# Kernel tuning notes

Hardware: AMD Instinct MI355X
Metric: run time of the kernel (lower is better)

Reference implementation:

```python
import jax, jax.numpy as jnp
import numpy as np

P = 16                     # patch size
D = 192                    # embed dim (forced by SAT d_model=192)
NHEAD = 3                  # ViT-Tiny heads
SAT_H, SAT_DK, SAT_DV = 8, 32, 32
N_SLICE = 10
PER_LI = jnp.linspace(0.1, 1.0, N_SLICE)
LN_EPS = 1e-5


def layernorm(z, g, b):
    m = z.mean(-1, keepdims=True)
    v = ((z - m) ** 2).mean(-1, keepdims=True)
    return (z - m) * jax.lax.rsqrt(v + LN_EPS) * g + b


def setup_inputs() -> dict:
    key = jax.random.key(0)
    ks = jax.random.split(key, 32)
    B, IMG, DEPTH, MLP = 128, 224, 12, 4 * D
    S = (IMG // P) ** 2 + 1  # 197 tokens
    n = lambda k, sh: jax.random.normal(k, sh, jnp.float32) * 0.02
    z = lambda sh: jnp.zeros(sh, jnp.float32)
    o = lambda sh: jnp.ones(sh, jnp.float32)
    return {
        "x": jax.random.uniform(ks[0], (B, 3, IMG, IMG), jnp.float32),
        "x_g_norm": jax.random.uniform(ks[1], (B, 1, 56, 56), jnp.float32),
        "patch_w": n(ks[2], (D, 3, P, P)), "patch_b": z((D,)),
        "cls_token": n(ks[3], (1, 1, D)), "pos_embed": n(ks[4], (1, S, D)),
        "eleva_embed": n(ks[5], (1, D)),
        "sat_wq": n(ks[6], (D, SAT_H * SAT_DK)), "sat_bq": z((SAT_H * SAT_DK,)),
        "sat_wk": n(ks[7], (D, SAT_H * SAT_DK)), "sat_bk": z((SAT_H * SAT_DK,)),
        "sat_wv": n(ks[8], (D, SAT_H * SAT_DV)), "sat_bv": z((SAT_H * SAT_DV,)),
        "sat_wo": n(ks[9], (SAT_H * SAT_DV, D)), "sat_bo": z((D,)),
        "ln1_g": o((DEPTH, D)), "ln1_b": z((DEPTH, D)),
        "qkv_w": n(ks[10], (DEPTH, D, 3 * D)), "qkv_b": z((DEPTH, 3 * D)),
        "proj_w": n(ks[11], (DEPTH, D, D)), "proj_b": z((DEPTH, D)),
        "ln2_g": o((DEPTH, D)), "ln2_b": z((DEPTH, D)),
        "fc1_w": n(ks[12], (DEPTH, D, MLP)), "fc1_b": z((DEPTH, MLP)),
        "fc2_w": n(ks[13], (DEPTH, MLP, D)), "fc2_b": z((DEPTH, D)),
        "norm_g": o((D,)), "norm_b": z((D,)),
    }


def _forward(x, x_g_norm, patch_w, patch_b, cls_token, pos_embed, eleva_embed,
             sat_wq, sat_bq, sat_wk, sat_bk, sat_wv, sat_bv, sat_wo, sat_bo,
             ln1_g, ln1_b, qkv_w, qkv_b, proj_w, proj_b, ln2_g, ln2_b,
             fc1_w, fc1_b, fc2_w, fc2_b, norm_g, norm_b):
    B = x.shape[0]
    # --- patch embed: Conv2d(3, D, kernel=P, stride=P) -> [B, N, D] ---
    feat = jax.lax.conv_general_dilated(
        x, patch_w, (P, P), 'VALID', dimension_numbers=('NCHW', 'OIHW', 'NCHW'))
    feat = feat + patch_b[None, :, None, None]
    tokens = feat.reshape(B, D, -1).transpose(0, 2, 1)          # [B, 196, D]
    tok = jnp.concatenate([jnp.broadcast_to(cls_token, (B, 1, D)), tokens], axis=1)
    tok = tok + pos_embed                                        # [B, S, D]
    S = tok.shape[1]
    # --- elevation weight per sample (vectorized bisect + linear interp) ---
    means = x_g_norm.mean(axis=(1, 2, 3))                        # [B]
    idx = jnp.clip(jnp.searchsorted(PER_LI, means, side='left'), 0, N_SLICE - 1)
    per_hi = PER_LI[idx]
    per_lo = jnp.where(idx == 0, 0.0, PER_LI[jnp.maximum(idx - 1, 0)])
    idx_f = idx.astype(jnp.float32)
    idx_inter = idx_f - (per_hi - means) / (per_hi - per_lo)
    w = jnp.where(idx == N_SLICE - 1, idx_f, idx_inter) / N_SLICE  # [B]
    # --- SAT fusion: per (batch, token) a 2-element attention over (token, ele) ---
    ele = jnp.broadcast_to(eleva_embed[0] * w[:, None, None], tok.shape)  # [B,S,D]
    at_in = jnp.stack([tok, ele], axis=2)                        # [B, S, 2, D]
    q = (at_in @ sat_wq + sat_bq).reshape(B, S, 2, SAT_H, SAT_DK)
    k = (at_in @ sat_wk + sat_bk).reshape(B, S, 2, SAT_H, SAT_DK)
    v = (at_in @ sat_wv + sat_bv).reshape(B, S, 2, SAT_H, SAT_DV)
    att = jnp.einsum('bsqhd,bskhd->bshqk', q, k) * (1.0 / np.sqrt(SAT_DK))
    att = jax.nn.softmax(att, axis=-1)
    sat_o = jnp.einsum('bshqk,bskhd->bsqhd', att, v).reshape(B, S, 2, SAT_H * SAT_DV)
    sat_o = sat_o @ sat_wo + sat_bo                              # [B, S, 2, D]
    h = sat_o[..., 0, :] + sat_o[..., 1, :]                      # [B, S, D]
    # --- ViT blocks via scan over stacked layer params ---
    hd = D // NHEAD

    def block(z, p):
        l1g, l1b, qw, qb, pw, pb, l2g, l2b, f1w, f1b, f2w, f2b = p
        y = layernorm(z, l1g, l1b)
        qkv = y @ qw + qb                                        # [B, S, 3D]
        q_, k_, v_ = jnp.split(qkv, 3, axis=-1)
        q_ = q_.reshape(B, S, NHEAD, hd)
        k_ = k_.reshape(B, S, NHEAD, hd)
        v_ = v_.reshape(B, S, NHEAD, hd)
        a = jnp.einsum('bqhd,bkhd->bhqk', q_, k_) * (hd ** -0.5)
        a = jax.nn.softmax(a, axis=-1)
        o = jnp.einsum('bhqk,bkhd->bqhd', a, v_).reshape(B, S, D)
        z = z + o @ pw + pb
        y = layernorm(z, l2g, l2b)
        z = z + jax.nn.gelu(y @ f1w + f1b, approximate=False) @ f2w + f2b
        return z, None

    h, _ = jax.lax.scan(block, h, (ln1_g, ln1_b, qkv_w, qkv_b, proj_w, proj_b,
                                   ln2_g, ln2_b, fc1_w, fc1_b, fc2_w, fc2_b))
    h = layernorm(h, norm_g, norm_b)
    return h[:, 0]                                               # [B, D] cls token


def reference(x, x_g_norm, patch_w, patch_b, cls_token, pos_embed, eleva_embed,
              sat_wq, sat_bq, sat_wk, sat_bk, sat_wv, sat_bv, sat_wo, sat_bo,
              ln1_g, ln1_b, qkv_w, qkv_b, proj_w, proj_b, ln2_g, ln2_b,
              fc1_w, fc1_b, fc2_w, fc2_b, norm_g, norm_b):
    return _forward(x, x_g_norm, patch_w, patch_b, cls_token, pos_embed, eleva_embed,
                    sat_wq, sat_bq, sat_wk, sat_bk, sat_wv, sat_bv, sat_wo, sat_bo,
                    ln1_g, ln1_b, qkv_w, qkv_b, proj_w, proj_b, ln2_g, ln2_b,
                    fc1_w, fc1_b, fc2_w, fc2_b, norm_g, norm_b)
```

## Files before the change

kernel.cpp:

```cpp
#include <hip/hip_runtime.h>


#define BATCH 128
#define SEQ 197
#define BS_ROWS (BATCH * SEQ)
#define DMODEL 192
#define NPATCH 196
#define MROWS_PATCH (BATCH * NPATCH)
#define KPATCH 768
#define MLPDIM 768
#define DEPTH 12
#define SPAD 224

typedef float f32x4 __attribute__((ext_vector_type(4)));
typedef short s16x8 __attribute__((ext_vector_type(8)));

__device__ __forceinline__ float wredSum(float v) {
#pragma unroll
  for (int o = 32; o > 0; o >>= 1) v += __shfl_xor(v, o, 64);
  return v;
}

__device__ __forceinline__ unsigned short f2bf(float f) {
  union { float f; unsigned u; } v;
  v.f = f;
  unsigned r = v.u + 0x7FFFu + ((v.u >> 16) & 1u);
  return (unsigned short)(r >> 16);
}
__device__ __forceinline__ float bf2f(unsigned short u) {
  union { unsigned u; float f; } v;
  v.u = ((unsigned)u) << 16;
  return v.f;
}

__global__ __launch_bounds__(256) void eleva_w_kernel(const float* __restrict__ xg,
                                                      float* __restrict__ wout) {
  const int b = blockIdx.x;
  const float* p = xg + (size_t)b * 3136;
  float s = 0.f;
  for (int i = threadIdx.x; i < 3136; i += 256) s += p[i];
  __shared__ float partial[4];
  s = wredSum(s);
  if ((threadIdx.x & 63) == 0) partial[threadIdx.x >> 6] = s;
  __syncthreads();
  if (threadIdx.x == 0) {
    float m = (partial[0] + partial[1] + partial[2] + partial[3]) / 3136.f;
    int idx = 0;
#pragma unroll
    for (int i = 0; i < 10; i++) {
      float pv = 0.1f * (float)(i + 1);
      if (pv < m) idx = i + 1;
    }
    if (idx > 9) idx = 9;
    float wv;
    if (idx == 9) {
      wv = 9.f;
    } else {
      float hi = 0.1f * (float)(idx + 1);
      float lo = (idx == 0) ? 0.f : 0.1f * (float)idx;
      wv = (float)idx - (hi - m) / (hi - lo);
    }
    wout[b] = wv / 10.f;
  }
}

__global__ __launch_bounds__(256) void wtrans_kernel(const float* __restrict__ in,
                                                     unsigned short* __restrict__ out,
                                                     int R, int C) {
  const int z = blockIdx.z;
  in += (size_t)z * R * C;
  out += (size_t)z * R * C;
  const int c0 = blockIdx.x * 32, r0 = blockIdx.y * 32;
  __shared__ float t[32][33];
  const int tr = threadIdx.x >> 3, tc = (threadIdx.x & 7) * 4;
  const float4 v = *(const float4*)(in + (size_t)(r0 + tr) * C + c0 + tc);
  t[tr][tc] = v.x; t[tr][tc + 1] = v.y; t[tr][tc + 2] = v.z; t[tr][tc + 3] = v.w;
  __syncthreads();
  ushort4 o;
  o.x = f2bf(t[tc + 0][tr]);
  o.y = f2bf(t[tc + 1][tr]);
  o.z = f2bf(t[tc + 2][tr]);
  o.w = f2bf(t[tc + 3][tr]);
  *(ushort4*)(out + (size_t)(c0 + tr) * R + r0 + tc) = o;
}

__global__ __launch_bounds__(256) void convert_kernel(const float* __restrict__ in,
                                                      unsigned short* __restrict__ out, int n4) {
  const int i = blockIdx.x * 256 + threadIdx.x;
  if (i >= n4) return;
  const float4 v = *(const float4*)(in + (size_t)i * 4);
  ushort4 o;
  o.x = f2bf(v.x); o.y = f2bf(v.y); o.z = f2bf(v.z); o.w = f2bf(v.w);
  *(ushort4*)(out + (size_t)i * 4) = o;
}

__global__ __launch_bounds__(256) void im2col_kernel(const float* __restrict__ x,
                                                     unsigned short* __restrict__ col) {
  const int i = blockIdx.x * 256 + threadIdx.x;
  if (i >= MROWS_PATCH * KPATCH / 8) return;
  const int k = (i % 96) * 8, row = i / 96;
  const int b = row / NPATCH, p = row % NPATCH;
  const int py = p / 14, px = p % 14;
  const int c = k >> 8, r = (k >> 4) & 15, cc = k & 15;
  const float* src = x + (((size_t)b * 3 + c) * 224 + (py * 16 + r)) * 224 + (px * 16 + cc);
  const float4 v0 = *(const float4*)src;
  const float4 v1 = *(const float4*)(src + 4);
  s16x8 o;
  o[0] = (short)f2bf(v0.x); o[1] = (short)f2bf(v0.y);
  o[2] = (short)f2bf(v0.z); o[3] = (short)f2bf(v0.w);
  o[4] = (short)f2bf(v1.x); o[5] = (short)f2bf(v1.y);
  o[6] = (short)f2bf(v1.z); o[7] = (short)f2bf(v1.w);
  *(s16x8*)(col + (size_t)i * 8) = o;
}

__global__ __launch_bounds__(256) void cls_kernel(const float* __restrict__ cls,
                                                  const float* __restrict__ pos,
                                                  float* __restrict__ H,
                                                  unsigned short* __restrict__ Hbf) {
  const int i = blockIdx.x * 256 + threadIdx.x;
  if (i >= BATCH * DMODEL) return;
  const int b = i / DMODEL, d = i % DMODEL;
  const float v = cls[d] + pos[d];
  const size_t idx = (size_t)b * SEQ * DMODEL + d;
  H[idx] = v;
  Hbf[idx] = f2bf(v);
}

__global__ __launch_bounds__(256) void ele_proj_kernel(
    const float* __restrict__ ele_emb, const float* __restrict__ wq, const float* __restrict__ bq,
    const float* __restrict__ wk, const float* __restrict__ bk,
    const float* __restrict__ wv, const float* __restrict__ bv,
    const float* __restrict__ wvec, float* __restrict__ eq, float* __restrict__ ek,
    float* __restrict__ ev, float* __restrict__ satb) {
  const int b = blockIdx.x, t = threadIdx.x;
  if (b == 0) {
    satb[t] = bq[t];
    satb[256 + t] = bk[t];
    satb[512 + t] = bv[t];
  }
  __shared__ float es[DMODEL];
  if (t < DMODEL) es[t] = ele_emb[t] * wvec[b];
  __syncthreads();
  float aq = bq[t], ak = bk[t], av = bv[t];
  for (int d = 0; d < DMODEL; d++) {
    const float e = es[d];
    aq += e * wq[d * 256 + t];
    ak += e * wk[d * 256 + t];
    av += e * wv[d * 256 + t];
  }
  eq[b * 256 + t] = aq;
  ek[b * 256 + t] = ak;
  ev[b * 256 + t] = av;
}

__global__ __launch_bounds__(256) void sat_mix_kernel(
    const unsigned short* __restrict__ qkv768, const float* __restrict__ eq,
    const float* __restrict__ ek, const float* __restrict__ ev,
    unsigned short* __restrict__ o256) {
  const int gid = blockIdx.x * 256 + threadIdx.x;
  const int tok = gid >> 3, h = gid & 7;
  if (tok >= BS_ROWS) return;
  const int b = tok / SEQ;
  const unsigned short* qp = qkv768 + (size_t)tok * 768 + h * 32;
  const unsigned short* kp = qp + 256;
  const unsigned short* vp = qp + 512;
  const float* eqp = eq + b * 256 + h * 32;
  const float* ekp = ek + b * 256 + h * 32;
  const float* evp = ev + b * 256 + h * 32;
  float s00 = 0.f, s01 = 0.f, s10 = 0.f, s11 = 0.f;
#pragma unroll 8
  for (int d = 0; d < 32; d++) {
    const float q_ = bf2f(qp[d]), k_ = bf2f(kp[d]), eq_ = eqp[d], ek_ = ekp[d];
    s00 += q_ * k_;
    s01 += q_ * ek_;
    s10 += eq_ * k_;
    s11 += eq_ * ek_;
  }
  const float sc = 0.17677669529663687f;
  s00 *= sc; s01 *= sc; s10 *= sc; s11 *= sc;
  const float m0 = fmaxf(s00, s01), m1 = fmaxf(s10, s11);
  const float e00 = __expf(s00 - m0), e01 = __expf(s01 - m0);
  const float e10 = __expf(s10 - m1), e11 = __expf(s11 - m1);
  const float w0 = e00 / (e00 + e01) + e10 / (e10 + e11);
  const float w1 = e01 / (e00 + e01) + e11 / (e10 + e11);
  unsigned short* op = o256 + (size_t)tok * 256 + h * 32;
#pragma unroll 8
  for (int d = 0; d < 32; d++) op[d] = f2bf(w0 * bf2f(vp[d]) + w1 * evp[d]);
}

template <int EPI>
__global__ __launch_bounds__(256) void gemm_mfma(const unsigned short* __restrict__ A,
                                                 const unsigned short* __restrict__ Bt,
                                                 const float* __restrict__ bias,
                                                 const float* __restrict__ res,
                                                 void* __restrict__ Cout,
                                                 unsigned short* __restrict__ aux_hbf,
                                                 const float* __restrict__ aux_pos,
                                                 int M, int N, int K) {
  __shared__ unsigned short As[2 * 128 * 64];
  __shared__ unsigned short Bs[2 * 96 * 64];
  const int tid = threadIdx.x, lane = tid & 63, w = tid >> 6;
  const int n0 = blockIdx.x * 96;
  const int m0 = blockIdx.y * 128;
  const int c = lane & 15, g = lane >> 4;
  const int wm = (w >> 1) * 64, wn = (w & 1) * 48;
  f32x4 acc[4][3] = {};

  auto stage = [&](int k0, int buf) {
#pragma unroll
    for (int it = 0; it < 4; it++) {
      const int s = it * 64 + lane;
      const int r = w * 32 + (s >> 3);
      const int scol = (s & 7) ^ (r & 7);
      const unsigned short* gp = A + (size_t)(m0 + r) * K + k0 + scol * 8;
      __builtin_amdgcn_global_load_lds(
          (const __attribute__((address_space(1))) unsigned int*)gp,
          (__attribute__((address_space(3))) unsigned int*)(As + buf * 8192 + w * 2048 + it * 512),
          16, 0, 0);
    }
#pragma unroll
    for (int it = 0; it < 3; it++) {
      const int s = it * 64 + lane;
      const int r = w * 24 + (s >> 3);
      const int scol = (s & 7) ^ (r & 7);
      const unsigned short* gp = Bt + (size_t)(n0 + r) * K + k0 + scol * 8;
      __builtin_amdgcn_global_load_lds(
          (const __attribute__((address_space(1))) unsigned int*)gp,
          (__attribute__((address_space(3))) unsigned int*)(Bs + buf * 6144 + w * 1536 + it * 512),
          16, 0, 0);
    }
  };

  auto compute = [&](int buf) {
#pragma unroll
    for (int kk = 0; kk < 2; kk++) {
      const int sw = (((kk * 4 + g) ^ (c & 7))) << 3;
      s16x8 af[4], bfr[3];
#pragma unroll
      for (int i = 0; i < 4; i++)
        af[i] = *(const s16x8*)&As[buf * 8192 + (wm + i * 16 + c) * 64 + sw];
#pragma unroll
      for (int j = 0; j < 3; j++)
        bfr[j] = *(const s16x8*)&Bs[buf * 6144 + (wn + j * 16 + c) * 64 + sw];
#pragma unroll
      for (int i = 0; i < 4; i++)
#pragma unroll
        for (int j = 0; j < 3; j++)
          acc[i][j] = __builtin_amdgcn_mfma_f32_16x16x32_bf16(af[i], bfr[j], acc[i][j], 0, 0, 0);
    }
  };

  int cur = 0;
  stage(0, 0);
  __syncthreads();
  for (int k0 = 64; k0 < K; k0 += 64) {
    stage(k0, cur ^ 1);
    compute(cur);
    __syncthreads();
    cur ^= 1;
  }
  compute(cur);

  const int ncol0 = n0 + wn + c;
  float bv[3];
#pragma unroll
  for (int j = 0; j < 3; j++) bv[j] = bias[ncol0 + j * 16] * (EPI == 3 ? 2.f : 1.f);
#pragma unroll
  for (int i = 0; i < 4; i++) {
#pragma unroll
    for (int r_ = 0; r_ < 4; r_++) {
      const int mrow = m0 + wm + i * 16 + g * 4 + r_;
      if (EPI == 4) {
        const int bb = mrow / 196;
        const int p = mrow - bb * 196;
        const size_t drow = (size_t)mrow + bb + 1;
#pragma unroll
        for (int j = 0; j < 3; j++) {
          const int col = ncol0 + j * 16;
          const float v = acc[i][j][r_] + bv[j] + aux_pos[(size_t)(p + 1) * DMODEL + col];
          const size_t idx = drow * DMODEL + col;
          ((float*)Cout)[idx] = v;
          aux_hbf[idx] = f2bf(v);
        }
      } else {
#pragma unroll
        for (int j = 0; j < 3; j++) {
          float v = acc[i][j][r_] + bv[j];
          const size_t idx = (size_t)mrow * N + ncol0 + j * 16;
          if (EPI == 0) {
            ((unsigned short*)Cout)[idx] = f2bf(v);
          } else if (EPI == 1) {
            v = 0.5f * v * (1.0f + erff(v * 0.70710678118654752f));
            ((unsigned short*)Cout)[idx] = f2bf(v);
          } else if (EPI == 2) {
            ((float*)Cout)[idx] = v + res[idx];
          } else {
            ((float*)Cout)[idx] = v;
          }
        }
      }
    }
  }
}

__global__ __launch_bounds__(256) void ln_kernel(const float* __restrict__ X,
                                                 const float* __restrict__ g,
                                                 const float* __restrict__ bta,
                                                 unsigned short* __restrict__ Y, int nrows) {
  const int w = threadIdx.x >> 6, lane = threadIdx.x & 63;
  const int row = blockIdx.x * 4 + w;
  if (row >= nrows) return;
  const float* x = X + (size_t)row * DMODEL;
  const float x0 = x[lane], x1 = x[lane + 64], x2 = x[lane + 128];
  const float m = wredSum(x0 + x1 + x2) * (1.f / 192.f);
  const float d0 = x0 - m, d1 = x1 - m, d2 = x2 - m;
  const float v = wredSum(d0 * d0 + d1 * d1 + d2 * d2) * (1.f / 192.f);
  const float inv = rsqrtf(v + 1e-5f);
  unsigned short* y = Y + (size_t)row * DMODEL;
  y[lane] = f2bf(d0 * inv * g[lane] + bta[lane]);
  y[lane + 64] = f2bf(d1 * inv * g[lane + 64] + bta[lane + 64]);
  y[lane + 128] = f2bf(d2 * inv * g[lane + 128] + bta[lane + 128]);
}

__global__ __launch_bounds__(256) void final_ln_kernel(const float* __restrict__ H,
                                                       const float* __restrict__ g,
                                                       const float* __restrict__ bta,
                                                       float* __restrict__ out) {
  const int w = threadIdx.x >> 6, lane = threadIdx.x & 63;
  const int bi = blockIdx.x * 4 + w;
  if (bi >= BATCH) return;
  const float* x = H + (size_t)bi * SEQ * DMODEL;
  const float x0 = x[lane], x1 = x[lane + 64], x2 = x[lane + 128];
  const float m = wredSum(x0 + x1 + x2) * (1.f / 192.f);
  const float d0 = x0 - m, d1 = x1 - m, d2 = x2 - m;
  const float v = wredSum(d0 * d0 + d1 * d1 + d2 * d2) * (1.f / 192.f);
  const float inv = rsqrtf(v + 1e-5f);
  float* y = out + (size_t)bi * DMODEL;
  y[lane] = d0 * inv * g[lane] + bta[lane];
  y[lane + 64] = d1 * inv * g[lane + 64] + bta[lane + 64];
  y[lane + 128] = d2 * inv * g[lane + 128] + bta[lane + 128];
}

__global__ __launch_bounds__(256) void vtrans_kernel(const unsigned short* __restrict__ qkv,
                                                     unsigned short* __restrict__ vt) {
  const int bid = blockIdx.x;
  const int sc = bid & 3, bh = bid >> 2;
  const int b = bh / 3, h = bh % 3;
  const int s0 = sc * 64;
  __shared__ unsigned short t[64][72];
  const int tid = threadIdx.x;
  for (int e = tid; e < 64 * 64; e += 256) {
    const int sp = e >> 6, d = e & 63;
    const int s = s0 + sp;
    t[sp][d] = (s < SEQ) ? qkv[((size_t)(b * SEQ + s)) * 576 + 384 + h * 64 + d] : (unsigned short)0;
  }
  __syncthreads();
  for (int e = tid; e < 64 * 64; e += 256) {
    const int d = e >> 6, sp = e & 63;
    const int s = s0 + sp;
    if (s < SPAD) vt[((size_t)bh * 64 + d) * SPAD + s] = t[sp][d];
  }
}

__global__ __launch_bounds__(64) void attn_mfma_kernel(const unsigned short* __restrict__ qkv,
                                                       const unsigned short* __restrict__ vt,
                                                       unsigned short* __restrict__ out) {
  const int bid = blockIdx.x;
  const int bh = bid / 13, qt = bid % 13;
  const int b = bh / 3, h = bh % 3;
  const int row0 = b * SEQ;
  const int q0 = qt * 16;
  const int lane = threadIdx.x;
  const int c = lane & 15, g = lane >> 4;

  __shared__ __attribute__((aligned(16))) unsigned short P[16][232];

  const int qr = row0 + min(q0 + c, SEQ - 1);
  const unsigned short* qp = qkv + (size_t)qr * 576 + h * 64 + g * 8;
  const s16x8 qlo = *(const s16x8*)qp;
  const s16x8 qhi = *(const s16x8*)(qp + 32);

  f32x4 acc[13];
#pragma unroll
  for (int t = 0; t < 13; t++) {
    const int kr = row0 + min(t * 16 + c, SEQ - 1);
    const unsigned short* kp = qkv + (size_t)kr * 576 + 192 + h * 64 + g * 8;
    const s16x8 klo = *(const s16x8*)kp;
    const s16x8 khi = *(const s16x8*)(kp + 32);
    f32x4 z = {0.f, 0.f, 0.f, 0.f};
    z = __builtin_amdgcn_mfma_f32_16x16x32_bf16(qlo, klo, z, 0, 0, 0);
    acc[t] = __builtin_amdgcn_mfma_f32_16x16x32_bf16(qhi, khi, z, 0, 0, 0);
  }

  const bool m12 = (c >= 5);
#pragma unroll
  for (int r = 0; r < 4; r++) {
    float mx = -INFINITY;
#pragma unroll
    for (int t = 0; t < 13; t++) {
      const float v = (t == 12 && m12) ? -INFINITY : acc[t][r];
      mx = fmaxf(mx, v);
    }
#pragma unroll
    for (int o = 1; o <= 8; o <<= 1) mx = fmaxf(mx, __shfl_xor(mx, o, 64));
    const float ms = mx * 0.125f;
    float sum = 0.f;
#pragma unroll
    for (int t = 0; t < 13; t++) {
      const float e = (t == 12 && m12) ? 0.f : __expf(acc[t][r] * 0.125f - ms);
      acc[t][r] = e;
      sum += e;
    }
#pragma unroll
    for (int o = 1; o <= 8; o <<= 1) sum += __shfl_xor(sum, o, 64);
    const float inv = 1.f / sum;
#pragma unroll
    for (int t = 0; t < 13; t++) P[g * 4 + r][t * 16 + c] = f2bf(acc[t][r] * inv);
  }
  {
    unsigned short z4[4] = {0, 0, 0, 0};
    *(uint2*)&P[c][208 + g * 4] = *(uint2*)z4;
  }
  __builtin_amdgcn_s_waitcnt(0);

  f32x4 oacc[4];
#pragma unroll
  for (int dt = 0; dt < 4; dt++) oacc[dt] = (f32x4){0.f, 0.f, 0.f, 0.f};
  const unsigned short* vbase = vt + (size_t)bh * 64 * SPAD;
#pragma unroll
  for (int ch = 0; ch < 7; ch++) {
    const s16x8 pa = *(const s16x8*)&P[c][ch * 32 + g * 8];
#pragma unroll
    for (int dt = 0; dt < 4; dt++) {
      const s16x8 vb = *(const s16x8*)(vbase + (size_t)(dt * 16 + c) * SPAD + ch * 32 + g * 8);
      oacc[dt] = __builtin_amdgcn_mfma_f32_16x16x32_bf16(pa, vb, oacc[dt], 0, 0, 0);
    }
  }

#pragma unroll
  for (int dt = 0; dt < 4; dt++) {
#pragma unroll
    for (int r = 0; r < 4; r++) {
      const int q = q0 + g * 4 + r;
      if (q < SEQ) out[(size_t)(row0 + q) * DMODEL + h * 64 + dt * 16 + c] = f2bf(oacc[dt][r]);
    }
  }
}

extern "C" void kernel_launch(void* const* d_in, const int* in_sizes, int n_in,
                              void* d_out, int out_size, void* d_ws, size_t ws_size,
                              hipStream_t stream) {
  const float* x       = (const float*)d_in[0];
  const float* xg      = (const float*)d_in[1];
  const float* patch_w = (const float*)d_in[2];
  const float* patch_b = (const float*)d_in[3];
  const float* cls_tok = (const float*)d_in[4];
  const float* pos_emb = (const float*)d_in[5];
  const float* ele_emb = (const float*)d_in[6];
  const float* sat_wq  = (const float*)d_in[7];
  const float* sat_bq  = (const float*)d_in[8];
  const float* sat_wk  = (const float*)d_in[9];
  const float* sat_bk  = (const float*)d_in[10];
  const float* sat_wv  = (const float*)d_in[11];
  const float* sat_bv  = (const float*)d_in[12];
  const float* sat_wo  = (const float*)d_in[13];
  const float* sat_bo  = (const float*)d_in[14];
  const float* ln1_g   = (const float*)d_in[15];
  const float* ln1_b   = (const float*)d_in[16];
  const float* qkv_w   = (const float*)d_in[17];
  const float* qkv_b   = (const float*)d_in[18];
  const float* proj_w  = (const float*)d_in[19];
  const float* proj_b  = (const float*)d_in[20];
  const float* ln2_g   = (const float*)d_in[21];
  const float* ln2_b   = (const float*)d_in[22];
  const float* fc1_w   = (const float*)d_in[23];
  const float* fc1_b   = (const float*)d_in[24];
  const float* fc2_w   = (const float*)d_in[25];
  const float* fc2_b   = (const float*)d_in[26];
  const float* norm_g  = (const float*)d_in[27];
  const float* norm_b  = (const float*)d_in[28];
  float* out = (float*)d_out;
  float* ws = (float*)d_ws;

  float* W_ELE = ws;
  float* EQ = ws + 256;
  float* EK = EQ + 32768;
  float* EV = EK + 32768;
  float* H = ws + 98560;
  unsigned short* Hbf   = (unsigned short*)(ws + 4940032);
  unsigned short* Ybf   = (unsigned short*)(ws + 7360768);
  unsigned short* QKVbf = (unsigned short*)(ws + 9781504);
  unsigned short* MLPbf = (unsigned short*)(ws + 17043712);
  unsigned short* VTB   = (unsigned short*)(ws + 26726656);
  unsigned short* WTS   = (unsigned short*)(ws + 29479168);
  float* SATB = ws + 32305408;

  unsigned short* qkv_wt   = WTS;
  unsigned short* proj_wt  = WTS + 1327104;
  unsigned short* fc1_wt   = WTS + 1769472;
  unsigned short* fc2_wt   = WTS + 3538944;
  unsigned short* patch_bf = WTS + 5308416;
  unsigned short* satqkv_t = WTS + 5455872;
  unsigned short* sato_t   = WTS + 5603328;

  unsigned short* COLbf   = MLPbf;
  unsigned short* SATQKV  = MLPbf;
  unsigned short* O256bf  = QKVbf;

  wtrans_kernel<<<dim3(18, 6, 12), 256, 0, stream>>>(qkv_w, qkv_wt, 192, 576);
  wtrans_kernel<<<dim3(6, 6, 12), 256, 0, stream>>>(proj_w, proj_wt, 192, 192);
  wtrans_kernel<<<dim3(24, 6, 12), 256, 0, stream>>>(fc1_w, fc1_wt, 192, 768);
  wtrans_kernel<<<dim3(6, 24, 12), 256, 0, stream>>>(fc2_w, fc2_wt, 768, 192);
  wtrans_kernel<<<dim3(8, 6, 1), 256, 0, stream>>>(sat_wq, satqkv_t, 192, 256);
  wtrans_kernel<<<dim3(8, 6, 1), 256, 0, stream>>>(sat_wk, satqkv_t + 49152, 192, 256);
  wtrans_kernel<<<dim3(8, 6, 1), 256, 0, stream>>>(sat_wv, satqkv_t + 98304, 192, 256);
  wtrans_kernel<<<dim3(6, 8, 1), 256, 0, stream>>>(sat_wo, sato_t, 256, 192);
  convert_kernel<<<144, 256, 0, stream>>>(patch_w, patch_bf, 36864);

  eleva_w_kernel<<<BATCH, 256, 0, stream>>>(xg, W_ELE);

  im2col_kernel<<<(MROWS_PATCH * KPATCH / 8) / 256, 256, 0, stream>>>(x, COLbf);
  gemm_mfma<4><<<dim3(2, 196), 256, 0, stream>>>(COLbf, patch_bf, patch_b, nullptr, H, Hbf,
                                                 pos_emb, MROWS_PATCH, DMODEL, KPATCH);
  cls_kernel<<<(BATCH * DMODEL) / 256, 256, 0, stream>>>(cls_tok, pos_emb, H, Hbf);

  ele_proj_kernel<<<BATCH, 256, 0, stream>>>(ele_emb, sat_wq, sat_bq, sat_wk, sat_bk,
                                             sat_wv, sat_bv, W_ELE, EQ, EK, EV, SATB);
  gemm_mfma<0><<<dim3(8, 197), 256, 0, stream>>>(Hbf, satqkv_t, SATB, nullptr, SATQKV,
                                                 nullptr, nullptr, BS_ROWS, 768, DMODEL);
  sat_mix_kernel<<<BS_ROWS / 32, 256, 0, stream>>>(SATQKV, EQ, EK, EV, O256bf);
  gemm_mfma<3><<<dim3(2, 197), 256, 0, stream>>>(O256bf, sato_t, sat_bo, nullptr, H,
                                                 nullptr, nullptr, BS_ROWS, DMODEL, 256);

  for (int l = 0; l < DEPTH; l++) {
    ln_kernel<<<BS_ROWS / 4, 256, 0, stream>>>(H, ln1_g + l * DMODEL, ln1_b + l * DMODEL, Ybf,
                                               BS_ROWS);
    gemm_mfma<0><<<dim3(6, 197), 256, 0, stream>>>(Ybf, qkv_wt + (size_t)l * 110592,
                                                   qkv_b + l * 576, nullptr, QKVbf, nullptr,
                                                   nullptr, BS_ROWS, 576, DMODEL);
    vtrans_kernel<<<BATCH * 3 * 4, 256, 0, stream>>>(QKVbf, VTB);
    attn_mfma_kernel<<<BATCH * 3 * 13, 64, 0, stream>>>(QKVbf, VTB, Ybf);
    gemm_mfma<2><<<dim3(2, 197), 256, 0, stream>>>(Ybf, proj_wt + (size_t)l * 36864,
                                                   proj_b + l * DMODEL, H, H, nullptr, nullptr,
                                                   BS_ROWS, DMODEL, DMODEL);
    ln_kernel<<<BS_ROWS / 4, 256, 0, stream>>>(H, ln2_g + l * DMODEL, ln2_b + l * DMODEL, Ybf,
                                               BS_ROWS);
    gemm_mfma<1><<<dim3(8, 197), 256, 0, stream>>>(Ybf, fc1_wt + (size_t)l * 147456,
                                                   fc1_b + l * MLPDIM, nullptr, MLPbf, nullptr,
                                                   nullptr, BS_ROWS, MLPDIM, DMODEL);
    gemm_mfma<2><<<dim3(2, 197), 256, 0, stream>>>(MLPbf, fc2_wt + (size_t)l * 147456,
                                                   fc2_b + l * DMODEL, H, H, nullptr, nullptr,
                                                   BS_ROWS, DMODEL, MLPDIM);
  }

  final_ln_kernel<<<BATCH / 4, 256, 0, stream>>>(H, norm_g, norm_b, out);
}
```

Measured before the change: 2.002 ms.

## Pre-swizzle GEMM operands in global memory and drop LDS double buffering

Every producer of a GEMM A or B operand (weight transposes, im2col, layernorm, attention output, SAT mix, fc1 epilogue, cls/patch writes) now stores bf16 rows with an XOR swizzle of the 8-element groups. The GEMM can then copy contiguous 16-byte chunks straight into LDS without computing the swizzle. The GEMM also drops to a single LDS buffer with launch_bounds(256,4), trading prefetch overlap for higher occupancy, and erff in the GELU epilogue is replaced by a polynomial erfc approximation. Risks: every consumer of these buffers must agree on the swizzled layout, the single buffer exposes load latency, and the GELU approximation has small error.

```diff
diff --git a/kernel.cpp b/kernel.cpp
--- a/kernel.cpp
+++ b/kernel.cpp
@@ -31,6 +31,24 @@
   union { unsigned u; float f; } v;
   v.u = ((unsigned)u) << 16;
   return v.f;
+}
+
+__device__ __forceinline__ int swz(int col, int row) {
+  int g8 = col >> 3;
+  g8 = (g8 & ~7) | ((g8 & 7) ^ (row & 7));
+  return (g8 << 3) | (col & 7);
+}
+
+__device__ __forceinline__ float gelu(float x) {
+  const float ax = fabsf(x) * 0.70710678118654752f;
+  const float t = 1.f / (1.f + 0.3275911f * ax);
+  const float y =
+      t * (0.254829592f +
+           t * (-0.284496736f +
+                t * (1.421413741f + t * (-1.453152027f + t * 1.061405429f))));
+  const float erfc_ = y * __expf(-ax * ax);
+  const float cdf = (x >= 0.f) ? (1.f - 0.5f * erfc_) : (0.5f * erfc_);
+  return x * cdf;
 }
 
 __global__ __launch_bounds__(256) void eleva_w_kernel(const float* __restrict__ xg,
@@ -81,17 +99,21 @@
   o.y = f2bf(t[tc + 1][tr]);
   o.z = f2bf(t[tc + 2][tr]);
   o.w = f2bf(t[tc + 3][tr]);
-  *(ushort4*)(out + (size_t)(c0 + tr) * R + r0 + tc) = o;
+  const int brow = c0 + tr;
+  *(ushort4*)(out + (size_t)brow * R + swz(r0 + tc, brow)) = o;
 }
 
 __global__ __launch_bounds__(256) void convert_kernel(const float* __restrict__ in,
-                                                      unsigned short* __restrict__ out, int n4) {
+                                                      unsigned short* __restrict__ out, int n4,
+                                                      int K) {
   const int i = blockIdx.x * 256 + threadIdx.x;
   if (i >= n4) return;
-  const float4 v = *(const float4*)(in + (size_t)i * 4);
+  const int flat = i * 4;
+  const int row = flat / K, col = flat % K;
+  const float4 v = *(const float4*)(in + flat);
   ushort4 o;
   o.x = f2bf(v.x); o.y = f2bf(v.y); o.z = f2bf(v.z); o.w = f2bf(v.w);
-  *(ushort4*)(out + (size_t)i * 4) = o;
+  *(ushort4*)(out + (size_t)row * K + swz(col, row)) = o;
 }
 
 __global__ __launch_bounds__(256) void im2col_kernel(const float* __restrict__ x,
@@ -110,7 +132,7 @@
   o[2] = (short)f2bf(v0.z); o[3] = (short)f2bf(v0.w);
   o[4] = (short)f2bf(v1.x); o[5] = (short)f2bf(v1.y);
   o[6] = (short)f2bf(v1.z); o[7] = (short)f2bf(v1.w);
-  *(s16x8*)(col + (size_t)i * 8) = o;
+  *(s16x8*)(col + (size_t)row * KPATCH + swz(k, row)) = o;
 }
 
 __global__ __launch_bounds__(256) void cls_kernel(const float* __restrict__ cls,
@@ -121,9 +143,9 @@
   if (i >= BATCH * DMODEL) return;
   const int b = i / DMODEL, d = i % DMODEL;
   const float v = cls[d] + pos[d];
-  const size_t idx = (size_t)b * SEQ * DMODEL + d;
-  H[idx] = v;
-  Hbf[idx] = f2bf(v);
+  const int row = b * SEQ;
+  H[(size_t)row * DMODEL + d] = v;
+  Hbf[(size_t)row * DMODEL + swz(d, row)] = f2bf(v);
 }
 
 __global__ __launch_bounds__(256) void ele_proj_kernel(
@@ -183,22 +205,23 @@
   const float e10 = __expf(s10 - m1), e11 = __expf(s11 - m1);
   const float w0 = e00 / (e00 + e01) + e10 / (e10 + e11);
   const float w1 = e01 / (e00 + e01) + e11 / (e10 + e11);
-  unsigned short* op = o256 + (size_t)tok * 256 + h * 32;
+  unsigned short* op = o256 + (size_t)tok * 256;
 #pragma unroll 8
-  for (int d = 0; d < 32; d++) op[d] = f2bf(w0 * bf2f(vp[d]) + w1 * evp[d]);
-}
-
-template <int EPI>
-__global__ __launch_bounds__(256) void gemm_mfma(const unsigned short* __restrict__ A,
-                                                 const unsigned short* __restrict__ Bt,
-                                                 const float* __restrict__ bias,
-                                                 const float* __restrict__ res,
-                                                 void* __restrict__ Cout,
-                                                 unsigned short* __restrict__ aux_hbf,
-                                                 const float* __restrict__ aux_pos,
-                                                 int M, int N, int K) {
-  __shared__ unsigned short As[2 * 128 * 64];
-  __shared__ unsigned short Bs[2 * 96 * 64];
+  for (int d = 0; d < 32; d++)
+    op[swz(h * 32 + d, tok)] = f2bf(w0 * bf2f(vp[d]) + w1 * evp[d]);
+}
+
+template <int EPI, bool SWZO>
+__global__ __launch_bounds__(256, 4) void gemm_mfma(const unsigned short* __restrict__ A,
+                                                    const unsigned short* __restrict__ Bt,
+                                                    const float* __restrict__ bias,
+                                                    const float* __restrict__ res,
+                                                    void* __restrict__ Cout,
+                                                    unsigned short* __restrict__ aux_hbf,
+                                                    const float* __restrict__ aux_pos,
+                                                    int M, int N, int K) {
+  __shared__ unsigned short As[128 * 64];
+  __shared__ unsigned short Bs[96 * 64];
   const int tid = threadIdx.x, lane = tid & 63, w = tid >> 6;
   const int n0 = blockIdx.x * 96;
   const int m0 = blockIdx.y * 128;
@@ -206,60 +229,47 @@
   const int wm = (w >> 1) * 64, wn = (w & 1) * 48;
   f32x4 acc[4][3] = {};
 
-  auto stage = [&](int k0, int buf) {
+  const int ar = (lane >> 3);
+  const int acol = (lane & 7) * 8;
+
+  for (int k0 = 0; k0 < K; k0 += 64) {
 #pragma unroll
     for (int it = 0; it < 4; it++) {
-      const int s = it * 64 + lane;
-      const int r = w * 32 + (s >> 3);
-      const int scol = (s & 7) ^ (r & 7);
-      const unsigned short* gp = A + (size_t)(m0 + r) * K + k0 + scol * 8;
+      const int r = w * 32 + it * 8 + ar;
+      const unsigned short* gp = A + (size_t)(m0 + r) * K + k0 + acol;
       __builtin_amdgcn_global_load_lds(
           (const __attribute__((address_space(1))) unsigned int*)gp,
-          (__attribute__((address_space(3))) unsigned int*)(As + buf * 8192 + w * 2048 + it * 512),
+          (__attribute__((address_space(3))) unsigned int*)(As + w * 2048 + it * 512),
           16, 0, 0);
     }
 #pragma unroll
     for (int it = 0; it < 3; it++) {
-      const int s = it * 64 + lane;
-      const int r = w * 24 + (s >> 3);
-      const int scol = (s & 7) ^ (r & 7);
-      const unsigned short* gp = Bt + (size_t)(n0 + r) * K + k0 + scol * 8;
+      const int r = w * 24 + it * 8 + ar;
+      const unsigned short* gp = Bt + (size_t)(n0 + r) * K + k0 + acol;
       __builtin_amdgcn_global_load_lds(
           (const __attribute__((address_space(1))) unsigned int*)gp,
-          (__attribute__((address_space(3))) unsigned int*)(Bs + buf * 6144 + w * 1536 + it * 512),
+          (__attribute__((address_space(3))) unsigned int*)(Bs + w * 1536 + it * 512),
           16, 0, 0);
     }
-  };
-
-  auto compute = [&](int buf) {
+    __syncthreads();
 #pragma unroll
     for (int kk = 0; kk < 2; kk++) {
       const int sw = (((kk * 4 + g) ^ (c & 7))) << 3;
       s16x8 af[4], bfr[3];
 #pragma unroll
       for (int i = 0; i < 4; i++)
-        af[i] = *(const s16x8*)&As[buf * 8192 + (wm + i * 16 + c) * 64 + sw];
+        af[i] = *(const s16x8*)&As[(wm + i * 16 + c) * 64 + sw];
 #pragma unroll
       for (int j = 0; j < 3; j++)
-        bfr[j] = *(const s16x8*)&Bs[buf * 6144 + (wn + j * 16 + c) * 64 + sw];
+        bfr[j] = *(const s16x8*)&Bs[(wn + j * 16 + c) * 64 + sw];
 #pragma unroll
       for (int i = 0; i < 4; i++)
 #pragma unroll
         for (int j = 0; j < 3; j++)
           acc[i][j] = __builtin_amdgcn_mfma_f32_16x16x32_bf16(af[i], bfr[j], acc[i][j], 0, 0, 0);
     }
-  };
-
-  int cur = 0;
-  stage(0, 0);
-  __syncthreads();
-  for (int k0 = 64; k0 < K; k0 += 64) {
-    stage(k0, cur ^ 1);
-    compute(cur);
     __syncthreads();
-    cur ^= 1;
-  }
-  compute(cur);
+  }
 
   const int ncol0 = n0 + wn + c;
   float bv[3];
@@ -273,29 +283,28 @@
       if (EPI == 4) {
         const int bb = mrow / 196;
         const int p = mrow - bb * 196;
-        const size_t drow = (size_t)mrow + bb + 1;
+        const int drow = mrow + bb + 1;
 #pragma unroll
         for (int j = 0; j < 3; j++) {
           const int col = ncol0 + j * 16;
           const float v = acc[i][j][r_] + bv[j] + aux_pos[(size_t)(p + 1) * DMODEL + col];
-          const size_t idx = drow * DMODEL + col;
-          ((float*)Cout)[idx] = v;
-          aux_hbf[idx] = f2bf(v);
+          ((float*)Cout)[(size_t)drow * DMODEL + col] = v;
+          aux_hbf[(size_t)drow * DMODEL + swz(col, drow)] = f2bf(v);
         }
       } else {
 #pragma unroll
         for (int j = 0; j < 3; j++) {
           float v = acc[i][j][r_] + bv[j];
-          const size_t idx = (size_t)mrow * N + ncol0 + j * 16;
+          const int col = ncol0 + j * 16;
+          const size_t rowoff = (size_t)mrow * N;
           if (EPI == 0) {
-            ((unsigned short*)Cout)[idx] = f2bf(v);
+            ((unsigned short*)Cout)[rowoff + (SWZO ? swz(col, mrow) : col)] = f2bf(v);
           } else if (EPI == 1) {
-            v = 0.5f * v * (1.0f + erff(v * 0.70710678118654752f));
-            ((unsigned short*)Cout)[idx] = f2bf(v);
+            ((unsigned short*)Cout)[rowoff + (SWZO ? swz(col, mrow) : col)] = f2bf(gelu(v));
           } else if (EPI == 2) {
-            ((float*)Cout)[idx] = v + res[idx];
+            ((float*)Cout)[rowoff + col] = v + res[rowoff + col];
           } else {
-            ((float*)Cout)[idx] = v;
+            ((float*)Cout)[rowoff + col] = v;
           }
         }
       }
@@ -317,9 +326,9 @@
   const float v = wredSum(d0 * d0 + d1 * d1 + d2 * d2) * (1.f / 192.f);
   const float inv = rsqrtf(v + 1e-5f);
   unsigned short* y = Y + (size_t)row * DMODEL;
-  y[lane] = f2bf(d0 * inv * g[lane] + bta[lane]);
-  y[lane + 64] = f2bf(d1 * inv * g[lane + 64] + bta[lane + 64]);
-  y[lane + 128] = f2bf(d2 * inv * g[lane + 128] + bta[lane + 128]);
+  y[swz(lane, row)] = f2bf(d0 * inv * g[lane] + bta[lane]);
+  y[swz(lane + 64, row)] = f2bf(d1 * inv * g[lane + 64] + bta[lane + 64]);
+  y[swz(lane + 128, row)] = f2bf(d2 * inv * g[lane + 128] + bta[lane + 128]);
 }
 
 __global__ __launch_bounds__(256) void final_ln_kernel(const float* __restrict__ H,
@@ -442,7 +451,10 @@
 #pragma unroll
     for (int r = 0; r < 4; r++) {
       const int q = q0 + g * 4 + r;
-      if (q < SEQ) out[(size_t)(row0 + q) * DMODEL + h * 64 + dt * 16 + c] = f2bf(oacc[dt][r]);
+      if (q < SEQ) {
+        const int trow = row0 + q;
+        out[(size_t)trow * DMODEL + swz(h * 64 + dt * 16 + c, trow)] = f2bf(oacc[dt][r]);
+      }
     }
   }
 }
@@ -515,42 +527,45 @@
   wtrans_kernel<<<dim3(8, 6, 1), 256, 0, stream>>>(sat_wk, satqkv_t + 49152, 192, 256);
   wtrans_kernel<<<dim3(8, 6, 1), 256, 0, stream>>>(sat_wv, satqkv_t + 98304, 192, 256);
   wtrans_kernel<<<dim3(6, 8, 1), 256, 0, stream>>>(sat_wo, sato_t, 256, 192);
-  convert_kernel<<<144, 256, 0, stream>>>(patch_w, patch_bf, 36864);
+  convert_kernel<<<144, 256, 0, stream>>>(patch_w, patch_bf, 36864, KPATCH);
 
   eleva_w_kernel<<<BATCH, 256, 0, stream>>>(xg, W_ELE);
 
   im2col_kernel<<<(MROWS_PATCH * KPATCH / 8) / 256, 256, 0, stream>>>(x, COLbf);
-  gemm_mfma<4><<<dim3(2, 196), 256, 0, stream>>>(COLbf, patch_bf, patch_b, nullptr, H, Hbf,
-                                                 pos_emb, MROWS_PATCH, DMODEL, KPATCH);
+  gemm_mfma<4, false><<<dim3(2, 196), 256, 0, stream>>>(COLbf, patch_bf, patch_b, nullptr, H,
+                                                        Hbf, pos_emb, MROWS_PATCH, DMODEL,
+                                                        KPATCH);
   cls_kernel<<<(BATCH * DMODEL) / 256, 256, 0, stream>>>(cls_tok, pos_emb, H, Hbf);
 
   ele_proj_kernel<<<BATCH, 256, 0, stream>>>(ele_emb, sat_wq, sat_bq, sat_wk, sat_bk,
                                              sat_wv, sat_bv, W_ELE, EQ, EK, EV, SATB);
-  gemm_mfma<0><<<dim3(8, 197), 256, 0, stream>>>(Hbf, satqkv_t, SATB, nullptr, SATQKV,
-                                                 nullptr, nullptr, BS_ROWS, 768, DMODEL);
+  gemm_mfma<0, false><<<dim3(8, 197), 256, 0, stream>>>(Hbf, satqkv_t, SATB, nullptr, SATQKV,
+                                                        nullptr, nullptr, BS_ROWS, 768, DMODEL);
   sat_mix_kernel<<<BS_ROWS / 32, 256, 0, stream>>>(SATQKV, EQ, EK, EV, O256bf);
-  gemm_mfma<3><<<dim3(2, 197), 256, 0, stream>>>(O256bf, sato_t, sat_bo, nullptr, H,
-                                                 nullptr, nullptr, BS_ROWS, DMODEL, 256);
+  gemm_mfma<3, false><<<dim3(2, 197), 256, 0, stream>>>(O256bf, sato_t, sat_bo, nullptr, H,
+                                                        nullptr, nullptr, BS_ROWS, DMODEL, 256);
 
   for (int l = 0; l < DEPTH; l++) {
     ln_kernel<<<BS_ROWS / 4, 256, 0, stream>>>(H, ln1_g + l * DMODEL, ln1_b + l * DMODEL, Ybf,
                                                BS_ROWS);
-    gemm_mfma<0><<<dim3(6, 197), 256, 0, stream>>>(Ybf, qkv_wt + (size_t)l * 110592,
-                                                   qkv_b + l * 576, nullptr, QKVbf, nullptr,
-                                                   nullptr, BS_ROWS, 576, DMODEL);
+    gemm_mfma<0, false><<<dim3(6, 197), 256, 0, stream>>>(Ybf, qkv_wt + (size_t)l * 110592,
+                                                          qkv_b + l * 576, nullptr, QKVbf,
+                                                          nullptr, nullptr, BS_ROWS, 576,
+                                                          DMODEL);
     vtrans_kernel<<<BATCH * 3 * 4, 256, 0, stream>>>(QKVbf, VTB);
     attn_mfma_kernel<<<BATCH * 3 * 13, 64, 0, stream>>>(QKVbf, VTB, Ybf);
-    gemm_mfma<2><<<dim3(2, 197), 256, 0, stream>>>(Ybf, proj_wt + (size_t)l * 36864,
-                                                   proj_b + l * DMODEL, H, H, nullptr, nullptr,
-                                                   BS_ROWS, DMODEL, DMODEL);
+    gemm_mfma<2, false><<<dim3(2, 197), 256, 0, stream>>>(Ybf, proj_wt + (size_t)l * 36864,
+                                                          proj_b + l * DMODEL, H, H, nullptr,
+                                                          nullptr, BS_ROWS, DMODEL, DMODEL);
     ln_kernel<<<BS_ROWS / 4, 256, 0, stream>>>(H, ln2_g + l * DMODEL, ln2_b + l * DMODEL, Ybf,
                                                BS_ROWS);
-    gemm_mfma<1><<<dim3(8, 197), 256, 0, stream>>>(Ybf, fc1_wt + (size_t)l * 147456,
-                                                   fc1_b + l * MLPDIM, nullptr, MLPbf, nullptr,
-                                                   nullptr, BS_ROWS, MLPDIM, DMODEL);
-    gemm_mfma<2><<<dim3(2, 197), 256, 0, stream>>>(MLPbf, fc2_wt + (size_t)l * 147456,
-                                                   fc2_b + l * DMODEL, H, H, nullptr, nullptr,
-                                                   BS_ROWS, DMODEL, MLPDIM);
+    gemm_mfma<1, true><<<dim3(8, 197), 256, 0, stream>>>(Ybf, fc1_wt + (size_t)l * 147456,
+                                                         fc1_b + l * MLPDIM, nullptr, MLPbf,
+                                                         nullptr, nullptr, BS_ROWS, MLPDIM,
+                                                         DMODEL);
+    gemm_mfma<2, false><<<dim3(2, 197), 256, 0, stream>>>(MLPbf, fc2_wt + (size_t)l * 147456,
+                                                          fc2_b + l * DMODEL, H, H, nullptr,
+                                                          nullptr, BS_ROWS, DMODEL, MLPDIM);
   }
 
   final_ln_kernel<<<BATCH / 4, 256, 0, stream>>>(H, norm_g, norm_b, out);
```

New measurement: 1.819 ms. 1.1x faster.
